# Performance work log

Measured on AMD Instinct MI355X. Metric: run time of the kernel, lower is better.

## Reference

```python
import jax, jax.numpy as jnp
import numpy as np

B, S, DIM = 2, 2048, 2048
N_HEADS, N_KV_HEADS = 16, 4
HEAD_DIM = DIM // N_HEADS  # 128
N_REP = N_HEADS // N_KV_HEADS
ROPE_THETA = 10000.0


def _rope_cos_sin(bsz, seqlen, head_dim, theta):
    # precompute_freqs_cis (unscaled): angles[t, i] = t * theta^{-2i/d}
    inv_freq = 1.0 / (theta ** (np.arange(0, head_dim, 2)[: head_dim // 2].astype(np.float32) / head_dim))
    t = np.arange(seqlen, dtype=np.float32)
    ang = np.outer(t, inv_freq)  # [S, hd/2]
    cos = np.broadcast_to(np.cos(ang), (bsz, seqlen, head_dim // 2))
    sin = np.broadcast_to(np.sin(ang), (bsz, seqlen, head_dim // 2))
    return jnp.asarray(cos), jnp.asarray(sin)


def setup_inputs() -> dict:
    key = jax.random.key(0)
    ks = jax.random.split(key, 5)
    scale = 1.0 / np.sqrt(DIM)
    x = jax.random.normal(ks[0], (B, S, DIM), dtype=jnp.float32)
    wq = jax.random.normal(ks[1], (DIM, N_HEADS * HEAD_DIM), dtype=jnp.float32) * scale
    wk = jax.random.normal(ks[2], (DIM, N_KV_HEADS * HEAD_DIM), dtype=jnp.float32) * scale
    wv = jax.random.normal(ks[3], (DIM, N_KV_HEADS * HEAD_DIM), dtype=jnp.float32) * scale
    wo = jax.random.normal(ks[4], (N_HEADS * HEAD_DIM, DIM), dtype=jnp.float32) * scale
    freqs_cos, freqs_sin = _rope_cos_sin(B, S, HEAD_DIM, ROPE_THETA)
    return {"x": x, "wq": wq, "wk": wk, "wv": wv, "wo": wo,
            "freqs_cos": freqs_cos, "freqs_sin": freqs_sin}


def _apply_rope(t, cos, sin):
    # t: [B, S, H, hd]; cos/sin: [B, S, hd/2] -> complex mult on (even, odd) pairs
    tr = t.reshape(*t.shape[:-1], -1, 2)  # [B,S,H,hd/2,2]
    xr, xi = tr[..., 0], tr[..., 1]
    c = cos[:, :, None, :]
    s = sin[:, :, None, :]
    out_r = xr * c - xi * s
    out_i = xr * s + xi * c
    return jnp.stack([out_r, out_i], axis=-1).reshape(t.shape)


def reference(x, wq, wk, wv, wo, freqs_cos, freqs_sin):
    bsz, seqlen, _ = x.shape
    xq = (x @ wq).reshape(bsz, seqlen, N_HEADS, HEAD_DIM)
    xk = (x @ wk).reshape(bsz, seqlen, N_KV_HEADS, HEAD_DIM)
    xv = (x @ wv).reshape(bsz, seqlen, N_KV_HEADS, HEAD_DIM)

    xq = _apply_rope(xq, freqs_cos, freqs_sin)
    xk = _apply_rope(xk, freqs_cos, freqs_sin)

    # repeat_kv (GQA): [B,S,KV,hd] -> [B,S,H,hd]
    xk = jnp.repeat(xk, N_REP, axis=2)
    xv = jnp.repeat(xv, N_REP, axis=2)

    # [B,H,Sq,Sk]
    scores = jnp.einsum('bqhd,bkhd->bhqk', xq, xk) / np.sqrt(HEAD_DIM).astype(np.float32)
    # additive causal mask (triu of -inf, diagonal=1)
    causal = jnp.triu(jnp.full((seqlen, seqlen), -jnp.inf, dtype=scores.dtype), k=1)
    scores = scores + causal
    probs = jax.nn.softmax(scores.astype(jnp.float32), axis=-1).astype(xq.dtype)
    out = jnp.einsum('bhqk,bkhd->bqhd', probs, xv).reshape(bsz, seqlen, -1)
    return out @ wo
```

## Files before the change

kernel.cpp:

```cpp
#include <hip/hip_runtime.h>
#include <stdint.h>

#define SEQ   2048
#define NB    2
#define LDQKV 3072
#define HD    128
#define QSCALE2 (0.08838834764831845f * 1.44269504088896340f)

typedef __attribute__((ext_vector_type(8))) short short8;
typedef __attribute__((ext_vector_type(4))) short short4v;
typedef __attribute__((ext_vector_type(4))) float f32x4;
typedef __attribute__((ext_vector_type(16))) float f32x16;
typedef __attribute__((ext_vector_type(4))) unsigned int u32x4;
typedef __attribute__((ext_vector_type(2))) unsigned int u32x2;
typedef __attribute__((ext_vector_type(8))) __bf16 bf16x8;

__device__ __forceinline__ float bs2f(short s) {
  unsigned int u = ((unsigned int)(unsigned short)s) << 16;
  return __builtin_bit_cast(float, u);
}
__device__ __forceinline__ short f2bs(float f) {
  unsigned int u = __builtin_bit_cast(unsigned int, f);
  u += 0x7fffu + ((u >> 16) & 1u);
  return (short)(u >> 16);
}
__device__ __forceinline__ unsigned int cvt_pk(float lo, float hi) {
  unsigned int r;
  asm("v_cvt_pk_bf16_f32 %0, %1, %2" : "=v"(r) : "v"(lo), "v"(hi));
  return r;
}
__device__ __forceinline__ float fexp2(float x) {
  float r;
  asm("v_exp_f32 %0, %1" : "=v"(r) : "v"(x));
  return r;
}
__device__ __forceinline__ f32x4 mfma16(short8 a, short8 b, f32x4 c) {
  return __builtin_amdgcn_mfma_f32_16x16x32_bf16(
      __builtin_bit_cast(bf16x8, a), __builtin_bit_cast(bf16x8, b), c, 0, 0, 0);
}
__device__ __forceinline__ f32x16 mfma32(short8 a, short8 b, f32x16 c) {
  return __builtin_amdgcn_mfma_f32_32x32x16_bf16(
      __builtin_bit_cast(bf16x8, a), __builtin_bit_cast(bf16x8, b), c, 0, 0, 0);
}
__device__ __forceinline__ void gload_lds16(const void* g, void* l) {
  __builtin_amdgcn_global_load_lds(
      (__attribute__((address_space(1))) const void*)(uintptr_t)g,
      (__attribute__((address_space(3))) void*)(unsigned int)(uintptr_t)l,
      16, 0, 0);
}

#define SBAR() asm volatile("s_barrier" ::: "memory")
#define VMC(n) asm volatile("s_waitcnt vmcnt(" #n ")" ::: "memory")

__global__ __launch_bounds__(256) void k_prep(const float* __restrict__ x,
                                              const float* __restrict__ wq,
                                              const float* __restrict__ wk,
                                              const float* __restrict__ wv,
                                              const float* __restrict__ wo,
                                              short* __restrict__ xb,
                                              short* __restrict__ wT,
                                              short* __restrict__ woT) {
  __shared__ __align__(16) float tile[64][68];
  const int bid = blockIdx.x, t = threadIdx.x;
  if (bid < 4096) {
    int i = bid * 256 + t;
    f32x4 a = *(const f32x4*)(x + (size_t)i * 8);
    f32x4 b = *(const f32x4*)(x + (size_t)i * 8 + 4);
    short8 o;
#pragma unroll
    for (int j = 0; j < 4; ++j) { o[j] = f2bs(a[j]); o[4 + j] = f2bs(b[j]); }
    *(short8*)(xb + (size_t)i * 8) = o;
    return;
  }
  const float* src;
  short* dst;
  int N, id;
  if (bid < 5120)      { id = bid - 4096; src = wq; dst = wT;                        N = 2048; }
  else if (bid < 5376) { id = bid - 5120; src = wk; dst = wT + (size_t)2048 * 2048;  N = 512;  }
  else if (bid < 5632) { id = bid - 5376; src = wv; dst = wT + (size_t)2560 * 2048;  N = 512;  }
  else                 { id = bid - 5632; src = wo; dst = woT;                       N = 2048; }
  const int K = 2048;
  int k0 = (id & 31) * 64, n0 = (id >> 5) * 64;
#pragma unroll
  for (int rep = 0; rep < 4; ++rep) {
    int lin = rep * 1024 + t * 4;
    int kk = lin >> 6, nn = lin & 63;
    f32x4 v = *(const f32x4*)(src + (size_t)(k0 + kk) * N + n0 + nn);
    *(f32x4*)(&tile[kk][nn]) = v;
  }
  __syncthreads();
#pragma unroll
  for (int rep = 0; rep < 4; ++rep) {
    int lin = rep * 1024 + t * 4;
    int nn = lin >> 6, kk = lin & 63;
    short4v o;
#pragma unroll
    for (int j = 0; j < 4; ++j) o[j] = f2bs(tile[kk + j][nn]);
    *(short4v*)(dst + (size_t)(n0 + nn) * K + k0 + kk) = o;
  }
}

template <int NH, int FP32OUT, int ROPE>
__global__ __launch_bounds__(512, 2) void k_gemm256(const short* __restrict__ A,
                                                    const short* __restrict__ Bt,
                                                    void* __restrict__ Cp,
                                                    const float* __restrict__ fcos,
                                                    const float* __restrict__ fsin,
                                                    int M, int N, int K) {
  __shared__ short Al[2][2][128 * 64];
  __shared__ short Bl[2][NH][128 * 64];
  const int t = threadIdx.x, l = t & 63, w = t >> 6;
  const int pm = w >> 2, pn = w & 3;
  const int lrow = l & 15, lg = l >> 4;
  const int NT = K >> 6;

  const int nbm = M >> 8;
  const int per = gridDim.x >> 3;
  const int id2 = (blockIdx.x & 7) * per + (blockIdx.x >> 3);
  const int m0 = (id2 % nbm) * 256, n0 = (id2 / nbm) * (NH * 128);

  const int srow = w * 8 + (l >> 3);
  const int sgx = ((l & 7) ^ (srow & 7)) * 8;
  const short* Abase = A + (size_t)(m0 + srow) * K + sgx;
  const short* Bbase = Bt + (size_t)(n0 + srow) * K + sgx;

  f32x4 acc[8][NH * 2] = {};
  short8 aFr0[4][2], aFr1[4][2], bFr[NH][2][2];

  auto stgA = [&](int d, int h, int tv) {
    const short* g = Abase + (size_t)(h * 128) * K + (size_t)tv * 64;
    gload_lds16(g, &Al[d][h][w * 512]);
    gload_lds16(g + (size_t)64 * K, &Al[d][h][w * 512 + 4096]);
  };
  auto stgB = [&](int d, int h, int tv) {
    const short* g = Bbase + (size_t)(h * 128) * K + (size_t)tv * 64;
    gload_lds16(g, &Bl[d][h][w * 512]);
    gload_lds16(g + (size_t)64 * K, &Bl[d][h][w * 512 + 4096]);
  };
  auto rdA = [&](int d, int Mh, short8 (*dst)[2]) {
#pragma unroll
    for (int mi = 0; mi < 4; ++mi) {
      int rl = pm * 64 + mi * 16 + lrow;
#pragma unroll
      for (int kk = 0; kk < 2; ++kk)
        dst[mi][kk] = *(const short8*)&Al[d][Mh][rl * 64 +
                                                 (((kk * 4 + lg) ^ (rl & 7)) * 8)];
    }
  };
  auto rdB = [&](int d) {
#pragma unroll
    for (int h = 0; h < NH; ++h)
#pragma unroll
      for (int ni = 0; ni < 2; ++ni) {
        int rl = pn * 32 + ni * 16 + lrow;
#pragma unroll
        for (int kk = 0; kk < 2; ++kk)
          bFr[h][ni][kk] =
              *(const short8*)&Bl[d][h][rl * 64 +
                                        (((kk * 4 + lg) ^ (rl & 7)) * 8)];
      }
  };

#define MMH(Mh, FR)                                                          \
  do {                                                                       \
    __builtin_amdgcn_s_setprio(1);                                           \
    _Pragma("unroll") for (int h = 0; h < NH; ++h)                           \
        _Pragma("unroll") for (int mi = 0; mi < 4; ++mi)                     \
            _Pragma("unroll") for (int ni = 0; ni < 2; ++ni)                 \
                _Pragma("unroll") for (int kk = 0; kk < 2; ++kk)             \
                    acc[(Mh)*4 + mi][h * 2 + ni] =                           \
                        mfma16(FR[mi][kk], bFr[h][ni][kk],                   \
                               acc[(Mh)*4 + mi][h * 2 + ni]);                \
    __builtin_amdgcn_s_setprio(0);                                           \
  } while (0)

  stgA(0, 0, 0);
  for (int h = 0; h < NH; ++h) stgB(0, h, 0);
  stgA(0, 1, 0);
  stgA(1, 0, 1);
  if (NH == 2) stgB(1, 1, 1);
  if (NH == 2) { VMC(4); } else { VMC(2); }
  SBAR();

  for (int v = 0; v < NT; ++v) {
    const int d = v & 1, d1 = d ^ 1;
    rdA(d, 0, aFr0);
    rdB(d);
    rdA(d, 1, aFr1);
    if (v + 1 < NT) { stgB(d1, 0, v + 1); stgA(d1, 1, v + 1); }
    MMH(0, aFr0);
    SBAR();
    if (v + 2 < NT) {
      stgA(d, 0, v + 2);
      if (NH == 2) stgB(d, 1, v + 2);
    }
    MMH(1, aFr1);
    if (v + 2 < NT) {
      if (NH == 2) { VMC(4); } else { VMC(2); }
    } else {
      VMC(0);
    }
    SBAR();
  }
#undef MMH

  const bool doRope = ROPE && (n0 < 2560);
  const float qs = (n0 < 2048) ? QSCALE2 : 1.0f;
  const int p0i = (pn * 32 + lrow) >> 1;
  const bool ev = ((lrow & 1) == 0);
#pragma unroll
  for (int Mh = 0; Mh < 2; ++Mh)
#pragma unroll
    for (int mi = 0; mi < 4; ++mi) {
      const int row = m0 + Mh * 128 + pm * 64 + mi * 16 + lg * 4;
      float cc[4][2], ss[4][2];
      if (doRope) {
#pragma unroll
        for (int v2 = 0; v2 < 4; ++v2)
#pragma unroll
          for (int ni = 0; ni < 2; ++ni) {
            cc[v2][ni] = fcos[(size_t)(row + v2) * 64 + p0i + ni * 8] * qs;
            ss[v2][ni] = fsin[(size_t)(row + v2) * 64 + p0i + ni * 8] * qs;
          }
      }
#pragma unroll
      for (int h = 0; h < NH; ++h)
#pragma unroll
        for (int ni = 0; ni < 2; ++ni) {
          int col = n0 + h * 128 + pn * 32 + ni * 16 + lrow;
          f32x4 vv = acc[Mh * 4 + mi][h * 2 + ni];
          if (doRope) {
#pragma unroll
            for (int v2 = 0; v2 < 4; ++v2) {
              float xx = vv[v2];
              float xp = __shfl_xor(xx, 1);
              vv[v2] = ev ? (xx * cc[v2][ni] - xp * ss[v2][ni])
                          : (xp * ss[v2][ni] + xx * cc[v2][ni]);
            }
          }
#pragma unroll
          for (int v2 = 0; v2 < 4; ++v2) {
            if constexpr (FP32OUT)
              ((float*)Cp)[(size_t)(row + v2) * N + col] = vv[v2];
            else
              ((short*)Cp)[(size_t)(row + v2) * N + col] = f2bs(vv[v2]);
          }
        }
    }
}

__global__ __launch_bounds__(256) void k_vt(const short* __restrict__ qkv,
                                            short* __restrict__ vt) {
  __shared__ short tile[128 * 137];
  const int id = blockIdx.x, t = threadIdx.x;
  int s0 = (id & 15) * 128;
  int kvh = (id >> 4) & 3, b = id >> 6;
  const short* src = qkv + (size_t)(b * SEQ) * LDQKV + 2560 + kvh * 128;
#pragma unroll
  for (int rep = 0; rep < 8; ++rep) {
    int lin = rep * 2048 + t * 8;
    int si = lin >> 7, d = lin & 127;
    short8 v = *(const short8*)(src + (size_t)(s0 + si) * LDQKV + d);
#pragma unroll
    for (int j = 0; j < 8; ++j) tile[si * 137 + d + j] = v[j];
  }
  __syncthreads();
  short* dst = vt + (size_t)((b * 4 + kvh) * 128) * SEQ;
#pragma unroll
  for (int rep = 0; rep < 8; ++rep) {
    int lin = rep * 2048 + t * 8;
    int d = lin >> 7, sb = lin & 127;
    short8 o;
#pragma unroll
    for (int j = 0; j < 8; ++j) o[j] = tile[(sb + j) * 137 + d];
    *(short8*)(dst + (size_t)d * SEQ + s0 + sb) = o;
  }
}

__global__ __launch_bounds__(256, 2) void k_attn(const short* __restrict__ qkv,
                                                 const short* __restrict__ vt,
                                                 short* __restrict__ outp) {
  __shared__ short Ks[2][64 * 128];
  __shared__ short Vs[2][128 * 64];
  const int t = threadIdx.x, l = t & 63, w = t >> 6;
  const int wr = w >> 1, wk = w & 1;
  const int h = blockIdx.y, b = blockIdx.z;
  const int kvh = h >> 2;
  const int lo5 = l & 31, hi = l >> 5;

  const int kkey = t >> 4, kd8 = t & 15;
  const int vdd = t >> 3, vs8 = t & 7;
  const short* kbase = qkv + (size_t)(b * SEQ) * LDQKV + 2048 + kvh * HD;
  const short* vbase = vt + (size_t)((b * 4 + kvh) * 128) * SEQ;

  auto stageKV = [&](int buf, int it) {
    const int kt = it * 64;
    short* kdst = &Ks[buf][w * 512];
    short* vdst = &Vs[buf][w * 512];
#pragma unroll
    for (int i = 0; i < 4; ++i) {
      int key = i * 16 + kkey;
      int sd = (kd8 ^ (key & 15)) * 8;
      gload_lds16(kbase + (size_t)(kt + key) * LDQKV + sd, kdst + i * 2048);
    }
#pragma unroll
    for (int i = 0; i < 4; ++i) {
      int d = i * 32 + vdd;
      int ss = (vs8 ^ (d & 7)) * 8;
      gload_lds16(vbase + (size_t)d * SEQ + kt + ss, vdst + i * 2048);
    }
  };

  int koff[8], voff[4][2];
#pragma unroll
  for (int s = 0; s < 8; ++s)
    koff[s] = (wk * 32 + lo5) * 128 + (((hi + 2 * s) ^ (l & 15)) * 8);
#pragma unroll
  for (int db = 0; db < 4; ++db)
#pragma unroll
    for (int s = 0; s < 2; ++s)
      voff[db][s] =
          (db * 32 + lo5) * 64 + (((4 * wk + hi + 2 * s) ^ (l & 7)) * 8);
  const int kbloc = wk * 32 + 4 * hi;
  const int qloc = wr * 32 + lo5;

  for (int part = 0; part < 2; ++part) {
    const int qt = part ? (31 - (int)blockIdx.x) : (int)blockIdx.x;
    const int q0 = qt * 64;

    short8 qf[8];
    {
      const short* qrow =
          qkv + (size_t)(b * SEQ + q0 + wr * 32 + lo5) * LDQKV + h * HD;
#pragma unroll
      for (int s = 0; s < 8; ++s)
        qf[s] = *(const short8*)(qrow + s * 16 + hi * 8);
    }

    f32x16 of[4] = {};
    float mrun = 0.f, lsum = 0.f;

    const int nt = qt + 1;
    stageKV(0, 0);
    __syncthreads();

    for (int it = 0; it < nt; ++it) {
      const int buf = it & 1;
      if (it + 1 < nt) stageKV(buf ^ 1, it + 1);
      const short* KsC = Ks[buf];
      const short* VsC = Vs[buf];

      f32x16 sca = {}, scb = {};
      __builtin_amdgcn_s_setprio(1);
#pragma unroll
      for (int s = 0; s < 4; ++s) {
        short8 kf0 = *(const short8*)(KsC + koff[2 * s]);
        short8 kf1 = *(const short8*)(KsC + koff[2 * s + 1]);
        sca = mfma32(kf0, qf[2 * s], sca);
        scb = mfma32(kf1, qf[2 * s + 1], scb);
      }
      __builtin_amdgcn_s_setprio(0);
      f32x16 sc = sca + scb;

      if (it == nt - 1) {
#pragma unroll
        for (int r = 0; r < 16; ++r) {
          const int off = (r & 3) + 8 * (r >> 2);
          if (kbloc + off > qloc) sc[r] = -1e30f;
        }
      }

      float lmax = sc[0];
#pragma unroll
      for (int r = 1; r < 16; ++r) lmax = fmaxf(lmax, sc[r]);
      if (__any(lmax > mrun + 8.f)) {
        float mx = fmaxf(lmax, __shfl_xor(lmax, 32));
        float mm = fmaxf(mrun, mx);
        float rs = fexp2(mrun - mm);
        mrun = mm;
        lsum *= rs;
#pragma unroll
        for (int db = 0; db < 4; ++db)
#pragma unroll
          for (int r = 0; r < 16; ++r) of[db][r] *= rs;
      }

      float p[16];
#pragma unroll
      for (int r = 0; r < 16; ++r) {
        p[r] = fexp2(sc[r] - mrun);
        lsum += p[r];
      }
      unsigned int pk[8];
#pragma unroll
      for (int j = 0; j < 8; ++j) pk[j] = cvt_pk(p[2 * j], p[2 * j + 1]);

      unsigned int s0 = hi ? pk[0] : pk[2];
      unsigned int s1 = hi ? pk[1] : pk[3];
      unsigned int s2 = hi ? pk[4] : pk[6];
      unsigned int s3 = hi ? pk[5] : pk[7];
      unsigned int x0 = __shfl_xor(s0, 32);
      unsigned int x1 = __shfl_xor(s1, 32);
      unsigned int x2 = __shfl_xor(s2, 32);
      unsigned int x3 = __shfl_xor(s3, 32);
      u32x4 b0w, b1w;
      b0w.x = hi ? x0 : pk[0];
      b0w.y = hi ? x1 : pk[1];
      b0w.z = hi ? pk[2] : x0;
      b0w.w = hi ? pk[3] : x1;
      b1w.x = hi ? x2 : pk[4];
      b1w.y = hi ? x3 : pk[5];
      b1w.z = hi ? pk[6] : x2;
      b1w.w = hi ? pk[7] : x3;
      short8 pb[2] = {__builtin_bit_cast(short8, b0w),
                      __builtin_bit_cast(short8, b1w)};

      __builtin_amdgcn_s_setprio(1);
#pragma unroll
      for (int s = 0; s < 2; ++s)
#pragma unroll
        for (int db = 0; db < 4; ++db) {
          short8 vf = *(const short8*)(VsC + voff[db][s]);
          of[db] = mfma32(vf, pb[s], of[db]);
        }
      __builtin_amdgcn_s_setprio(0);
      __syncthreads();
    }

    lsum += __shfl_xor(lsum, 32);
    float* og = (float*)Ks;
    float* sg = (float*)Vs;
    if (wk == 1) {
#pragma unroll
      for (int db = 0; db < 4; ++db)
#pragma unroll
        for (int r4 = 0; r4 < 4; ++r4) {
          int g = db * 4 + r4;
          f32x4 v;
#pragma unroll
          for (int j = 0; j < 4; ++j) v[j] = of[db][r4 * 4 + j];
          *(f32x4*)&og[wr * 4096 + l * 64 + ((g ^ (l & 15)) * 4)] = v;
        }
      sg[wr * 64 + l] = mrun;
      sg[128 + wr * 64 + l] = lsum;
    }
    __syncthreads();
    if (wk == 0) {
      float m1 = sg[wr * 64 + l];
      float l1 = sg[128 + wr * 64 + l];
      float mt = fmaxf(mrun, m1);
      float r0 = fexp2(mrun - mt), r1 = fexp2(m1 - mt);
      float inv = 1.0f / (lsum * r0 + l1 * r1);
      short* ob =
          outp + (size_t)(b * SEQ + q0 + wr * 32 + lo5) * 2048 + h * HD;
#pragma unroll
      for (int db = 0; db < 4; ++db) {
#pragma unroll
        for (int r4 = 0; r4 < 4; ++r4) {
          int g = db * 4 + r4;
          f32x4 o1 = *(const f32x4*)&og[wr * 4096 + l * 64 +
                                        ((g ^ (l & 15)) * 4)];
          u32x2 pko;
          float v0 = (of[db][r4 * 4 + 0] * r0 + o1[0] * r1) * inv;
          float v1 = (of[db][r4 * 4 + 1] * r0 + o1[1] * r1) * inv;
          float v2 = (of[db][r4 * 4 + 2] * r0 + o1[2] * r1) * inv;
          float v3 = (of[db][r4 * 4 + 3] * r0 + o1[3] * r1) * inv;
          pko.x = cvt_pk(v0, v1);
          pko.y = cvt_pk(v2, v3);
          *(u32x2*)(ob + db * 32 + 8 * r4 + 4 * hi) = pko;
        }
      }
    }
    __syncthreads();
  }
}

extern "C" void kernel_launch(void* const* d_in, const int* in_sizes, int n_in,
                              void* d_out, int out_size, void* d_ws,
                              size_t ws_size, hipStream_t stream) {
  const float* x = (const float*)d_in[0];
  const float* wq = (const float*)d_in[1];
  const float* wk = (const float*)d_in[2];
  const float* wv = (const float*)d_in[3];
  const float* wo = (const float*)d_in[4];
  const float* fc = (const float*)d_in[5];
  const float* fs = (const float*)d_in[6];

  char* ws = (char*)d_ws;
  short* xb = (short*)(ws);
  short* wT = (short*)(ws + (16ull << 20));
  short* woT = (short*)(ws + (28ull << 20));
  short* qkvb = (short*)(ws + (36ull << 20));
  short* vtb = (short*)(ws + (16ull << 20));
  short* attn = (short*)(ws);

  k_prep<<<6656, 256, 0, stream>>>(x, wq, wk, wv, wo, xb, wT, woT);
  k_gemm256<2, 0, 1><<<192, 512, 0, stream>>>(xb, wT, qkvb, fc, fs,
                                              4096, 3072, 2048);
  k_vt<<<128, 256, 0, stream>>>(qkvb, vtb);
  k_attn<<<dim3(16, 16, 2), 256, 0, stream>>>(qkvb, vtb, attn);
  k_gemm256<1, 1, 0><<<256, 512, 0, stream>>>(attn, woT, d_out, nullptr,
                                              nullptr, 4096, 2048, 2048);
}
```

Before: 180.2 us.

## Add dedicated 128x384-tile QKV projection GEMM to fill all 256 CUs

Replaces the 256x256 QKV projection GEMM (192 blocks) with a new kernel using 128x384 tiles, launched as 256 blocks so the grid matches the 256 compute units. RoPE and the Q scale are applied per 16-column fragment in the epilogue, and the RoPE path is removed from the generic GEMM template. The aim is to avoid the partial second wave or idle CUs of the 192-block grid. In exchange the smaller M tile gives less A reuse and more B traffic per block.

```diff
diff --git a/kernel.cpp b/kernel.cpp
--- a/kernel.cpp
+++ b/kernel.cpp
@@ -100,6 +100,125 @@
   }
 }
 
+__global__ __launch_bounds__(512, 2) void k_gemmQ(const short* __restrict__ A,
+                                                  const short* __restrict__ Bt,
+                                                  short* __restrict__ Cp,
+                                                  const float* __restrict__ fcos,
+                                                  const float* __restrict__ fsin) {
+  __shared__ short Al[2][128 * 64];
+  __shared__ short Bl[2][384 * 64];
+  const int t = threadIdx.x, l = t & 63, w = t >> 6;
+  const int pm = w >> 2, pn = w & 3;
+  const int lrow = l & 15, lg = l >> 4;
+  const int K = 2048, NT = 32;
+
+  const int id2 = ((int)blockIdx.x & 7) * 32 + ((int)blockIdx.x >> 3);
+  const int m0 = (id2 & 31) * 128, n0 = (id2 >> 5) * 384;
+
+  const int srow = w * 8 + (l >> 3);
+  const int sgx = ((l & 7) ^ (srow & 7)) * 8;
+  const short* Abase = A + (size_t)(m0 + srow) * K + sgx;
+  const short* Bbase = Bt + (size_t)(n0 + srow) * K + sgx;
+
+  f32x4 acc[4][6] = {};
+  short8 aFr[4][2], bFr[6][2];
+
+  auto stgA = [&](int d, int tv) {
+#pragma unroll
+    for (int j = 0; j < 2; ++j)
+      gload_lds16(Abase + (size_t)(j * 64) * K + (size_t)tv * 64,
+                  &Al[d][j * 4096 + w * 512]);
+  };
+  auto stgB = [&](int d, int tv) {
+#pragma unroll
+    for (int j = 0; j < 6; ++j)
+      gload_lds16(Bbase + (size_t)(j * 64) * K + (size_t)tv * 64,
+                  &Bl[d][j * 4096 + w * 512]);
+  };
+  auto rdA = [&](int d) {
+#pragma unroll
+    for (int mi = 0; mi < 4; ++mi) {
+      int rl = pm * 64 + mi * 16 + lrow;
+#pragma unroll
+      for (int kk = 0; kk < 2; ++kk)
+        aFr[mi][kk] = *(const short8*)&Al[d][rl * 64 +
+                                             (((kk * 4 + lg) ^ (rl & 7)) * 8)];
+    }
+  };
+  auto rdB = [&](int d) {
+#pragma unroll
+    for (int ni = 0; ni < 6; ++ni) {
+      int rl = pn * 96 + ni * 16 + lrow;
+#pragma unroll
+      for (int kk = 0; kk < 2; ++kk)
+        bFr[ni][kk] = *(const short8*)&Bl[d][rl * 64 +
+                                             (((kk * 4 + lg) ^ (rl & 7)) * 8)];
+    }
+  };
+
+  stgA(0, 0);
+  stgB(0, 0);
+  stgA(1, 1);
+  VMC(2);
+  SBAR();
+
+  for (int v = 0; v < NT; ++v) {
+    const int d = v & 1, d1 = d ^ 1;
+    if (v + 1 < NT) stgB(d1, v + 1);
+    rdA(d);
+    rdB(d);
+    __builtin_amdgcn_s_setprio(1);
+#pragma unroll
+    for (int mi = 0; mi < 4; ++mi)
+#pragma unroll
+      for (int ni = 0; ni < 3; ++ni)
+#pragma unroll
+        for (int kk = 0; kk < 2; ++kk)
+          acc[mi][ni] = mfma16(aFr[mi][kk], bFr[ni][kk], acc[mi][ni]);
+    __builtin_amdgcn_s_setprio(0);
+    SBAR();
+    if (v + 2 < NT) stgA(d, v + 2);
+    __builtin_amdgcn_s_setprio(1);
+#pragma unroll
+    for (int mi = 0; mi < 4; ++mi)
+#pragma unroll
+      for (int ni = 3; ni < 6; ++ni)
+#pragma unroll
+        for (int kk = 0; kk < 2; ++kk)
+          acc[mi][ni] = mfma16(aFr[mi][kk], bFr[ni][kk], acc[mi][ni]);
+    __builtin_amdgcn_s_setprio(0);
+    if (v + 2 < NT) { VMC(2); } else { VMC(0); }
+    SBAR();
+  }
+
+  const bool ev = ((lrow & 1) == 0);
+#pragma unroll
+  for (int mi = 0; mi < 4; ++mi) {
+    const int row = m0 + pm * 64 + mi * 16 + lg * 4;
+#pragma unroll
+    for (int ni = 0; ni < 6; ++ni) {
+      const int colb = n0 + pn * 96 + ni * 16;
+      const int col = colb + lrow;
+      f32x4 vv = acc[mi][ni];
+      if (colb < 2560) {
+        const float qs = (colb < 2048) ? QSCALE2 : 1.0f;
+        const int pi = ((pn * 96 + ni * 16 + lrow) & 127) >> 1;
+#pragma unroll
+        for (int v2 = 0; v2 < 4; ++v2) {
+          float c = fcos[(size_t)(row + v2) * 64 + pi] * qs;
+          float s = fsin[(size_t)(row + v2) * 64 + pi] * qs;
+          float xx = vv[v2];
+          float xp = __shfl_xor(xx, 1);
+          vv[v2] = ev ? (xx * c - xp * s) : (xp * s + xx * c);
+        }
+      }
+#pragma unroll
+      for (int v2 = 0; v2 < 4; ++v2)
+        Cp[(size_t)(row + v2) * LDQKV + col] = f2bs(vv[v2]);
+    }
+  }
+}
+
 template <int NH, int FP32OUT, int ROPE>
 __global__ __launch_bounds__(512, 2) void k_gemm256(const short* __restrict__ A,
                                                     const short* __restrict__ Bt,
@@ -204,40 +323,17 @@
   }
 #undef MMH
 
-  const bool doRope = ROPE && (n0 < 2560);
-  const float qs = (n0 < 2048) ? QSCALE2 : 1.0f;
-  const int p0i = (pn * 32 + lrow) >> 1;
-  const bool ev = ((lrow & 1) == 0);
 #pragma unroll
   for (int Mh = 0; Mh < 2; ++Mh)
 #pragma unroll
     for (int mi = 0; mi < 4; ++mi) {
       const int row = m0 + Mh * 128 + pm * 64 + mi * 16 + lg * 4;
-      float cc[4][2], ss[4][2];
-      if (doRope) {
-#pragma unroll
-        for (int v2 = 0; v2 < 4; ++v2)
-#pragma unroll
-          for (int ni = 0; ni < 2; ++ni) {
-            cc[v2][ni] = fcos[(size_t)(row + v2) * 64 + p0i + ni * 8] * qs;
-            ss[v2][ni] = fsin[(size_t)(row + v2) * 64 + p0i + ni * 8] * qs;
-          }
-      }
 #pragma unroll
       for (int h = 0; h < NH; ++h)
 #pragma unroll
         for (int ni = 0; ni < 2; ++ni) {
           int col = n0 + h * 128 + pn * 32 + ni * 16 + lrow;
           f32x4 vv = acc[Mh * 4 + mi][h * 2 + ni];
-          if (doRope) {
-#pragma unroll
-            for (int v2 = 0; v2 < 4; ++v2) {
-              float xx = vv[v2];
-              float xp = __shfl_xor(xx, 1);
-              vv[v2] = ev ? (xx * cc[v2][ni] - xp * ss[v2][ni])
-                          : (xp * ss[v2][ni] + xx * cc[v2][ni]);
-            }
-          }
 #pragma unroll
           for (int v2 = 0; v2 < 4; ++v2) {
             if constexpr (FP32OUT)
@@ -495,8 +591,7 @@
   short* attn = (short*)(ws);
 
   k_prep<<<6656, 256, 0, stream>>>(x, wq, wk, wv, wo, xb, wT, woT);
-  k_gemm256<2, 0, 1><<<192, 512, 0, stream>>>(xb, wT, qkvb, fc, fs,
-                                              4096, 3072, 2048);
+  k_gemmQ<<<256, 512, 0, stream>>>(xb, wT, qkvb, fc, fs);
   k_vt<<<128, 256, 0, stream>>>(qkvb, vtb);
   k_attn<<<dim3(16, 16, 2), 256, 0, stream>>>(qkvb, vtb, attn);
   k_gemm256<1, 1, 0><<<256, 512, 0, stream>>>(attn, woT, d_out, nullptr,
```

Result: faster. 174.8 us (-3.0%).
